# Kernel optimization log

Measured on AMD Instinct MI355X. Metric: run time of the kernel, lower is better.

Reference implementation:

```python
import jax, jax.numpy as jnp
import numpy as np

H2 = 450
W = 1242
H = 375
N_PTS = 4_000_000


def setup_inputs() -> dict:
    key = jax.random.key(0)
    k1, k2, k3, k4, k5 = jax.random.split(key, 5)
    # lidar point cloud in velodyne frame (homogeneous): x forward, y left, z up
    u = jax.random.uniform(k1, (N_PTS, 3), dtype=jnp.float32)
    x = u[:, 0] * 78.0 + 2.0           # 2..80 m forward
    y = (u[:, 1] - 0.5) * 40.0         # -20..20 m lateral
    z = (u[:, 2] - 0.5) * 4.0 - 1.0    # -3..1 m vertical
    velo = jnp.stack([x, y, z, jnp.ones_like(x)], axis=1)
    # KITTI-like padded 4x4 intrinsic
    intrinsic = jnp.array([[721.5, 0.0, 609.5, 0.0],
                           [0.0, 721.5, 172.8, 0.0],
                           [0.0, 0.0, 1.0, 0.0],
                           [0.0, 0.0, 0.0, 1.0]], dtype=jnp.float32)
    # cam extrinsic ~ identity with small stereo baseline translation
    camExtrinsic = jnp.eye(4, dtype=jnp.float32).at[0, 3].set(-0.06)
    # velodyne -> camera rigid transform
    R = jnp.array([[0.0, -1.0, 0.0],
                   [0.0, 0.0, -1.0],
                   [1.0, 0.0, 0.0]], dtype=jnp.float32)
    t = jnp.array([0.0, -0.08, -0.27], dtype=jnp.float32)
    lidarExtrinsic = jnp.eye(4, dtype=jnp.float32).at[:3, :3].set(R).at[:3, 3].set(t)
    d = jax.random.uniform(k2, (H2, W), dtype=jnp.float32) * 78.0 + 2.0
    sel = jax.random.uniform(k3, (H2, W), dtype=jnp.float32) > 0.3
    interp_depth = jnp.where(sel, d, 0.0)
    return {"velo": velo, "intrinsic": intrinsic, "camExtrinsic": camExtrinsic,
            "lidarExtrinsic": lidarExtrinsic, "interp_depth": interp_depth,
            "h": H, "w": W}


def reference(velo, intrinsic, camExtrinsic, lidarExtrinsic, interp_depth, h, w):
    h2, wd = interp_depth.shape
    n = velo.shape[0]
    f32 = interp_depth.dtype

    P_cam = intrinsic @ camExtrinsic      # 4x4 projection to camera image
    P_lid = intrinsic @ lidarExtrinsic    # 4x4 projection to lidar image

    # project points into camera image
    vp = velo @ P_cam.T                    # [N,4]
    vz = vp[:, 2]
    vx = vp[:, 0] / vz
    vy = vp[:, 1] / vz
    onimg = (velo[:, 0] > 0) & (vx > 0) & (vx < w) & (vy > 0) & (vy < h)

    # project points into lidar image
    nv = velo @ P_lid.T                    # [N,4]
    nz = nv[:, 2]
    nx = nv[:, 0] / nz
    ny = nv[:, 1] / nz
    rnx = jnp.round(nx).astype(jnp.int32)
    rny = jnp.round(ny).astype(jnp.int32)
    nval = (rnx >= 0) & (rnx < w) & (rny >= 0) & (rny < h2) & (nz > 0) & onimg

    # dense interp-depth backprojection / reprojection, [h2, w]
    xxx, yyy = jnp.meshgrid(jnp.arange(wd, dtype=f32), jnp.arange(h2, dtype=f32), indexing='xy')
    d = interp_depth
    pts = jnp.stack([xxx * d, yyy * d, d, jnp.ones_like(d)], axis=-1)  # [h2,w,4]
    M = P_cam @ jnp.linalg.inv(P_lid)
    pp = jnp.einsum('hwk,jk->hwj', pts, M)                              # [h2,w,4]
    ppz = pp[..., 2]
    ppz_safe = jnp.where(ppz != 0, ppz, 1.0)
    ppx = pp[..., 0] / ppz_safe
    ppy = pp[..., 1] / ppz_safe
    interp_vals = jnp.stack([xxx, yyy, d, ppx, ppy, ppz, jnp.zeros_like(d)], axis=-1)
    img = jnp.where((d > 0)[..., None], interp_vals, 0.0)               # [h2,w,7]

    # scatter lidar points (overwrites interp entries where both present)
    idxrec = jnp.arange(n, dtype=f32)
    pvals = jnp.stack([nx, ny, nz, vx, vy, vz, idxrec], axis=1)         # [N,7]
    y_safe = jnp.where(nval, rny, h2)                                   # OOB -> dropped
    img = img.at[y_safe, rnx].set(pvals, mode='drop')

    org_mask = jnp.zeros((h2, wd), dtype=f32).at[y_safe, rnx].set(1.0, mode='drop')
    # NOTE: the custom CUDA occlusion pass (LidarFilterCuda.lidar_denoise) is
    # not reproducible; reference keeps the pre-denoise mask (identity filter).
    noocc_mask = org_mask

    pt_idx = img[:, :, 6].astype(jnp.int32)
    keep = noocc_mask == 1
    fi_idx = jnp.where(keep, pt_idx, n)                                 # OOB -> dropped
    filterIndicator = jnp.zeros((n,), dtype=jnp.int32).at[fi_idx.reshape(-1)].set(1, mode='drop')

    return img, noocc_mask, org_mask, filterIndicator
```

## Files before the change

kernel.cpp:

```cpp
#include <hip/hip_runtime.h>

#define H2C 450
#define WC 1242
#define HC 375
#define NPTS 4000000
#define NPIX (H2C * WC)
#define TPB 256


__device__ __forceinline__ void mm4(float* o, const float* a, const float* b) {
#pragma unroll
    for (int i = 0; i < 4; i++)
#pragma unroll
        for (int j = 0; j < 4; j++) {
            float t = a[i * 4 + 0] * b[0 * 4 + j];
            t = fmaf(a[i * 4 + 1], b[1 * 4 + j], t);
            t = fmaf(a[i * 4 + 2], b[2 * 4 + j], t);
            t = fmaf(a[i * 4 + 3], b[3 * 4 + j], t);
            o[i * 4 + j] = t;
        }
}

__device__ void compute_mats(const float* K, const float* C, const float* L, float* out48) {
#pragma clang fp contract(off)
    float Pc[16], Pl[16], A[16], X[16], M[16];
    int piv[4];
    mm4(Pc, K, C);
    mm4(Pl, K, L);
#pragma unroll
    for (int k = 0; k < 16; k++) A[k] = Pl[k];

#pragma unroll
    for (int k = 0; k < 4; k++) {
        int p = k; float mx = fabsf(A[k * 4 + k]);
#pragma unroll
        for (int r = k + 1; r < 4; r++) {
            float v = fabsf(A[r * 4 + k]);
            if (v > mx) { mx = v; p = r; }
        }
        piv[k] = p;
#pragma unroll
        for (int r = k + 1; r < 4; r++) {
            bool sw = (p == r);
#pragma unroll
            for (int j = 0; j < 4; j++) {
                float tk = A[k * 4 + j], tr = A[r * 4 + j];
                A[k * 4 + j] = sw ? tr : tk;
                A[r * 4 + j] = sw ? tk : tr;
            }
        }
        float akk = A[k * 4 + k];
        if (fabsf(akk) >= 1.17549435e-38f) {
            float rr = 1.0f / akk;
#pragma unroll
            for (int r2 = k + 1; r2 < 4; r2++) A[r2 * 4 + k] = A[r2 * 4 + k] * rr;
        } else {
#pragma unroll
            for (int r2 = k + 1; r2 < 4; r2++) A[r2 * 4 + k] = A[r2 * 4 + k] / akk;
        }
#pragma unroll
        for (int r = k + 1; r < 4; r++) {
            float lik = A[r * 4 + k];
#pragma unroll
            for (int j = k + 1; j < 4; j++) A[r * 4 + j] = A[r * 4 + j] - lik * A[k * 4 + j];
        }
    }

#pragma unroll
    for (int k = 0; k < 16; k++) X[k] = 0.0f;
    X[0] = X[5] = X[10] = X[15] = 1.0f;
#pragma unroll
    for (int k = 0; k < 4; k++) {
        int p = piv[k];
#pragma unroll
        for (int r = k + 1; r < 4; r++) {
            bool sw = (p == r);
#pragma unroll
            for (int j = 0; j < 4; j++) {
                float tk = X[k * 4 + j], tr = X[r * 4 + j];
                X[k * 4 + j] = sw ? tr : tk;
                X[r * 4 + j] = sw ? tk : tr;
            }
        }
    }
#pragma unroll
    for (int j = 0; j < 4; j++) {
#pragma unroll
        for (int k = 0; k < 4; k++) {
            float xk = X[k * 4 + j];
#pragma unroll
            for (int r = k + 1; r < 4; r++) X[r * 4 + j] = X[r * 4 + j] - xk * A[r * 4 + k];
        }
#pragma unroll
        for (int k = 3; k >= 0; k--) {
            float xk = X[k * 4 + j] / A[k * 4 + k];
            X[k * 4 + j] = xk;
#pragma unroll
            for (int r = 0; r < k; r++) X[r * 4 + j] = X[r * 4 + j] - xk * A[r * 4 + k];
        }
    }
    mm4(M, Pc, X);
#pragma unroll
    for (int k = 0; k < 16; k++) { out48[k] = Pc[k]; out48[16 + k] = Pl[k]; out48[32 + k] = M[k]; }
}

__global__ void init_mats_k(const float* __restrict__ K, const float* __restrict__ C,
                            const float* __restrict__ L, float* __restrict__ gmats,
                            int4* __restrict__ winner4) {
    int i = blockIdx.x * blockDim.x + threadIdx.x;
    if (i < NPIX / 4) winner4[i] = make_int4(-1, -1, -1, -1);
    if (i == 0) compute_mats(K, C, L, gmats);
}

__global__ void point_k(const float4* __restrict__ velo, const float* __restrict__ mats,
                        int* __restrict__ winner, float* __restrict__ fi) {
    int i = blockIdx.x * blockDim.x + threadIdx.x;
    if (i >= NPTS) return;
    fi[i] = 0.0f;
    float4 v = velo[i];
    const float* Pc = mats;
    const float* Pl = mats + 16;
    float vp0 = fmaf(v.w, Pc[3],  fmaf(v.z, Pc[2],  fmaf(v.y, Pc[1], v.x * Pc[0])));
    float vp1 = fmaf(v.w, Pc[7],  fmaf(v.z, Pc[6],  fmaf(v.y, Pc[5], v.x * Pc[4])));
    float vz  = fmaf(v.w, Pc[11], fmaf(v.z, Pc[10], fmaf(v.y, Pc[9], v.x * Pc[8])));
    float vx = vp0 / vz;
    float vy = vp1 / vz;
    bool onimg = (v.x > 0.f) && (vx > 0.f) && (vx < (float)WC) && (vy > 0.f) && (vy < (float)HC);
    float nv0 = fmaf(v.w, Pl[3],  fmaf(v.z, Pl[2],  fmaf(v.y, Pl[1], v.x * Pl[0])));
    float nv1 = fmaf(v.w, Pl[7],  fmaf(v.z, Pl[6],  fmaf(v.y, Pl[5], v.x * Pl[4])));
    float nz  = fmaf(v.w, Pl[11], fmaf(v.z, Pl[10], fmaf(v.y, Pl[9], v.x * Pl[8])));
    float nx = nv0 / nz;
    float ny = nv1 / nz;
    float rx = rintf(nx);
    float ry = rintf(ny);
    if (onimg && (nz > 0.f) && (rx >= 0.f) && (rx < (float)WC) && (ry >= 0.f) && (ry < (float)H2C)) {
        int px = (int)rx, py = (int)ry;
        atomicMax(&winner[py * WC + px], i);
    }
}

__global__ void __launch_bounds__(TPB)
resolve_k(const float* __restrict__ depth, const float4* __restrict__ velo,
          const float* __restrict__ mats, const int* __restrict__ winner,
          float* __restrict__ img, float* __restrict__ noocc,
          float* __restrict__ org, float* __restrict__ fi) {
#pragma clang fp contract(off)
    __shared__ float srec[TPB * 7];
    int pb = blockIdx.x * TPB;
    int p = pb + threadIdx.x;
    int valid = NPIX - pb; if (valid > TPB) valid = TPB;
    float o0 = 0.f, o1 = 0.f, o2 = 0.f, o3 = 0.f, o4 = 0.f, o5 = 0.f, o6 = 0.f;
    if (p < NPIX) {
        int wi = winner[p];
        if (wi >= 0) {
            float4 v = velo[wi];
            const float* Pc = mats;
            const float* Pl = mats + 16;
            float vp0 = fmaf(v.w, Pc[3],  fmaf(v.z, Pc[2],  fmaf(v.y, Pc[1], v.x * Pc[0])));
            float vp1 = fmaf(v.w, Pc[7],  fmaf(v.z, Pc[6],  fmaf(v.y, Pc[5], v.x * Pc[4])));
            float vz  = fmaf(v.w, Pc[11], fmaf(v.z, Pc[10], fmaf(v.y, Pc[9], v.x * Pc[8])));
            float nv0 = fmaf(v.w, Pl[3],  fmaf(v.z, Pl[2],  fmaf(v.y, Pl[1], v.x * Pl[0])));
            float nv1 = fmaf(v.w, Pl[7],  fmaf(v.z, Pl[6],  fmaf(v.y, Pl[5], v.x * Pl[4])));
            float nz  = fmaf(v.w, Pl[11], fmaf(v.z, Pl[10], fmaf(v.y, Pl[9], v.x * Pl[8])));
            o0 = nv0 / nz; o1 = nv1 / nz; o2 = nz;
            o3 = vp0 / vz; o4 = vp1 / vz; o5 = vz;
            o6 = (float)wi;
            noocc[p] = 1.0f;
            org[p] = 1.0f;
            fi[wi] = 1.0f;
        } else {
            noocc[p] = 0.0f;
            org[p] = 0.0f;
            float d = depth[p];
            if (d > 0.0f) {
                int y = p / WC, x = p - y * WC;
                float fx = (float)x, fy = (float)y;
                const float* M = mats + 32;
                float p0 = fx * d, p1 = fy * d;
                float pp0 = ((p0 * M[0] + p1 * M[1]) + d * M[2]) + M[3];
                float pp1 = ((p0 * M[4] + p1 * M[5]) + d * M[6]) + M[7];
                float pp2 = ((p0 * M[8] + p1 * M[9]) + d * M[10]) + M[11];
                float zs = (pp2 != 0.0f) ? pp2 : 1.0f;
                o0 = fx; o1 = fy; o2 = d;
                o3 = pp0 / zs; o4 = pp1 / zs; o5 = pp2;
                o6 = 0.0f;
            }
        }
    }
    float* r = srec + threadIdx.x * 7;
    r[0] = o0; r[1] = o1; r[2] = o2; r[3] = o3; r[4] = o4; r[5] = o5; r[6] = o6;
    __syncthreads();
    float* obase = img + (size_t)pb * 7;
    int nfl = valid * 7;
    for (int k = threadIdx.x; k < nfl; k += TPB) obase[k] = srec[k];
}

extern "C" void kernel_launch(void* const* d_in, const int* in_sizes, int n_in,
                              void* d_out, int out_size, void* d_ws, size_t ws_size,
                              hipStream_t stream) {
    const float* velo  = (const float*)d_in[0];
    const float* K     = (const float*)d_in[1];
    const float* C     = (const float*)d_in[2];
    const float* L     = (const float*)d_in[3];
    const float* depth = (const float*)d_in[4];

    float* out   = (float*)d_out;
    float* img   = out;
    float* noocc = out + (size_t)NPIX * 7;
    float* org   = noocc + NPIX;
    float* fi    = org + NPIX;

    float* gmats = (float*)d_ws;
    int* winner  = (int*)((char*)d_ws + 256);

    init_mats_k<<<(NPIX / 4 + TPB - 1) / TPB, TPB, 0, stream>>>(K, C, L, gmats, (int4*)winner);

    point_k<<<(NPTS + TPB - 1) / TPB, TPB, 0, stream>>>((const float4*)velo, gmats, winner, fi);

    resolve_k<<<(NPIX + TPB - 1) / TPB, TPB, 0, stream>>>(depth, (const float4*)velo, gmats, winner,
                                                          img, noocc, org, fi);
}
```

Measured before the change: 29.05 us.

## Fold matrix setup into point kernel, memset winners, use grid-stride loop

Removes the separate init kernel. The winner buffer is now cleared with hipMemsetAsync, and every block of the point kernel computes the projection matrices redundantly into shared memory, with block 0 writing them out for the resolve kernel. The point kernel becomes a persistent grid-stride loop over 2048 blocks, and the matrix entries are hoisted into registers. This cuts one launch and the global matrix loads, but each block pays a serial single-thread LU inverse before it can start.

```diff
diff --git a/kernel.cpp b/kernel.cpp
--- a/kernel.cpp
+++ b/kernel.cpp
@@ -6,6 +6,8 @@
 #define NPTS 4000000
 #define NPIX (H2C * WC)
 #define TPB 256
+#define PBLK 2048
+#define PTHREADS (PBLK * TPB)
 
 
 __device__ __forceinline__ void mm4(float* o, const float* a, const float* b) {
@@ -104,38 +106,42 @@
     for (int k = 0; k < 16; k++) { out48[k] = Pc[k]; out48[16 + k] = Pl[k]; out48[32 + k] = M[k]; }
 }
 
-__global__ void init_mats_k(const float* __restrict__ K, const float* __restrict__ C,
-                            const float* __restrict__ L, float* __restrict__ gmats,
-                            int4* __restrict__ winner4) {
-    int i = blockIdx.x * blockDim.x + threadIdx.x;
-    if (i < NPIX / 4) winner4[i] = make_int4(-1, -1, -1, -1);
-    if (i == 0) compute_mats(K, C, L, gmats);
-}
-
-__global__ void point_k(const float4* __restrict__ velo, const float* __restrict__ mats,
-                        int* __restrict__ winner, float* __restrict__ fi) {
-    int i = blockIdx.x * blockDim.x + threadIdx.x;
-    if (i >= NPTS) return;
-    fi[i] = 0.0f;
-    float4 v = velo[i];
-    const float* Pc = mats;
-    const float* Pl = mats + 16;
-    float vp0 = fmaf(v.w, Pc[3],  fmaf(v.z, Pc[2],  fmaf(v.y, Pc[1], v.x * Pc[0])));
-    float vp1 = fmaf(v.w, Pc[7],  fmaf(v.z, Pc[6],  fmaf(v.y, Pc[5], v.x * Pc[4])));
-    float vz  = fmaf(v.w, Pc[11], fmaf(v.z, Pc[10], fmaf(v.y, Pc[9], v.x * Pc[8])));
-    float vx = vp0 / vz;
-    float vy = vp1 / vz;
-    bool onimg = (v.x > 0.f) && (vx > 0.f) && (vx < (float)WC) && (vy > 0.f) && (vy < (float)HC);
-    float nv0 = fmaf(v.w, Pl[3],  fmaf(v.z, Pl[2],  fmaf(v.y, Pl[1], v.x * Pl[0])));
-    float nv1 = fmaf(v.w, Pl[7],  fmaf(v.z, Pl[6],  fmaf(v.y, Pl[5], v.x * Pl[4])));
-    float nz  = fmaf(v.w, Pl[11], fmaf(v.z, Pl[10], fmaf(v.y, Pl[9], v.x * Pl[8])));
-    float nx = nv0 / nz;
-    float ny = nv1 / nz;
-    float rx = rintf(nx);
-    float ry = rintf(ny);
-    if (onimg && (nz > 0.f) && (rx >= 0.f) && (rx < (float)WC) && (ry >= 0.f) && (ry < (float)H2C)) {
-        int px = (int)rx, py = (int)ry;
-        atomicMax(&winner[py * WC + px], i);
+__global__ void __launch_bounds__(TPB, 4)
+point_k(const float4* __restrict__ velo, const float* __restrict__ K,
+        const float* __restrict__ C, const float* __restrict__ L,
+        int* __restrict__ winner, float* __restrict__ fi, float* __restrict__ gmats) {
+    __shared__ float smats[48];
+    if (threadIdx.x == 0) compute_mats(K, C, L, smats);
+    __syncthreads();
+    if (blockIdx.x == 0 && threadIdx.x < 48) gmats[threadIdx.x] = smats[threadIdx.x];
+    float pc0 = smats[0],  pc1 = smats[1],  pc2 = smats[2],  pc3 = smats[3];
+    float pc4 = smats[4],  pc5 = smats[5],  pc6 = smats[6],  pc7 = smats[7];
+    float pc8 = smats[8],  pc9 = smats[9],  pc10 = smats[10], pc11 = smats[11];
+    float pl0 = smats[16], pl1 = smats[17], pl2 = smats[18], pl3 = smats[19];
+    float pl4 = smats[20], pl5 = smats[21], pl6 = smats[22], pl7 = smats[23];
+    float pl8 = smats[24], pl9 = smats[25], pl10 = smats[26], pl11 = smats[27];
+
+    int tid = blockIdx.x * TPB + threadIdx.x;
+    for (int i = tid; i < NPTS; i += PTHREADS) {
+        fi[i] = 0.0f;
+        float4 v = velo[i];
+        float vp0 = fmaf(v.w, pc3,  fmaf(v.z, pc2,  fmaf(v.y, pc1, v.x * pc0)));
+        float vp1 = fmaf(v.w, pc7,  fmaf(v.z, pc6,  fmaf(v.y, pc5, v.x * pc4)));
+        float vz  = fmaf(v.w, pc11, fmaf(v.z, pc10, fmaf(v.y, pc9, v.x * pc8)));
+        float vx = vp0 / vz;
+        float vy = vp1 / vz;
+        bool onimg = (v.x > 0.f) && (vx > 0.f) && (vx < (float)WC) && (vy > 0.f) && (vy < (float)HC);
+        float nv0 = fmaf(v.w, pl3,  fmaf(v.z, pl2,  fmaf(v.y, pl1, v.x * pl0)));
+        float nv1 = fmaf(v.w, pl7,  fmaf(v.z, pl6,  fmaf(v.y, pl5, v.x * pl4)));
+        float nz  = fmaf(v.w, pl11, fmaf(v.z, pl10, fmaf(v.y, pl9, v.x * pl8)));
+        float nx = nv0 / nz;
+        float ny = nv1 / nz;
+        float rx = rintf(nx);
+        float ry = rintf(ny);
+        if (onimg && (nz > 0.f) && (rx >= 0.f) && (rx < (float)WC) && (ry >= 0.f) && (ry < (float)H2C)) {
+            int px = (int)rx, py = (int)ry;
+            atomicMax(&winner[py * WC + px], i);
+        }
     }
 }
 
@@ -213,9 +219,9 @@
     float* gmats = (float*)d_ws;
     int* winner  = (int*)((char*)d_ws + 256);
 
-    init_mats_k<<<(NPIX / 4 + TPB - 1) / TPB, TPB, 0, stream>>>(K, C, L, gmats, (int4*)winner);
-
-    point_k<<<(NPTS + TPB - 1) / TPB, TPB, 0, stream>>>((const float4*)velo, gmats, winner, fi);
+    hipMemsetAsync(winner, 0xFF, (size_t)NPIX * sizeof(int), stream);
+
+    point_k<<<PBLK, TPB, 0, stream>>>((const float4*)velo, K, C, L, winner, fi, gmats);
 
     resolve_k<<<(NPIX + TPB - 1) / TPB, TPB, 0, stream>>>(depth, (const float4*)velo, gmats, winner,
                                                           img, noocc, org, fi);
```

Result: slower. 34.47 us (+18.6%).
